# Kernel tuning notes

Measured on AMD Instinct MI355X. Metric: run time of the kernel, lower is better.

The kernel has to match this reference:

```python
import jax, jax.numpy as jnp
import numpy as np

N = 1024
C = 50000
D = 128
M_MARGIN = 0.35
S_SCALE = 30.0
LAMDA = 0.01


def setup_inputs() -> dict:
    key = jax.random.key(0)
    k1, k2, k3 = jax.random.split(key, 3)
    feature = jax.random.normal(k1, (N, D), dtype=jnp.float32)
    weight = jax.random.normal(k2, (C, D), dtype=jnp.float32)
    label = jax.random.randint(k3, (N,), 0, C, dtype=jnp.int64)
    return {"feature": feature, "weight": weight, "label": label}


def reference(feature, weight, label):
    eps = 1e-8  # torch CosineSimilarity eps
    f = feature / jnp.maximum(jnp.linalg.norm(feature, axis=-1, keepdims=True), eps)
    w = weight / jnp.maximum(jnp.linalg.norm(weight, axis=-1, keepdims=True), eps)
    cos = jnp.einsum("nd,cd->nc", f, w)  # [N, C] cosine similarities
    onehot = jax.nn.one_hot(label, C, dtype=cos.dtype)  # [N, C]
    # CosFace: subtract margin m from the target-class cosine, scale by s
    logits = S_SCALE * (cos - M_MARGIN * onehot)
    target_logit = S_SCALE * (jnp.take_along_axis(cos, label[:, None], axis=1)[:, 0] - M_MARGIN)
    # -log( exp(t) / (exp(t) + sum_{j != y} exp(s*cos_j)) ) = logsumexp(logits) - t
    lse = jax.nn.logsumexp(logits, axis=-1)  # [N]
    loss_lmc = jnp.mean(lse - target_logit)
    # center loss: 0.5 * sum_i ||f_i - w_{y_i}||^2
    diff = feature - weight[label]
    loss_c = 0.5 * jnp.sum(diff * diff)
    return loss_lmc + LAMDA * loss_c
```

## Files before the change

kernel.cpp:

```cpp
#include <hip/hip_runtime.h>

#define N_ROWS   1024
#define D_DIM    128
#define C_CLS    50000
#define C_PAD    50048
#define NCT64    782
#define NG       128
#define NPART    256
#define S_SCALE  30.0f
#define M_MARGIN 0.35f
#define EXP2_SCALE 43.2808512266689f
#define EXP2M      15.1482979293341f
#define LN2        0.6931471805599453f

typedef short s8v __attribute__((ext_vector_type(8)));
typedef float f4v __attribute__((ext_vector_type(4)));

__device__ inline unsigned short f2bf(float f) {
    unsigned u = __float_as_uint(f);
    u += 0x7FFF + ((u >> 16) & 1);
    return (unsigned short)(u >> 16);
}
__device__ inline float bf2f(unsigned short h) {
    return __uint_as_float(((unsigned)h) << 16);
}
__device__ inline void load_lds16(const char* src, unsigned char* lds) {
    __builtin_amdgcn_global_load_lds(
        (const __attribute__((address_space(1))) void*)src,
        (__attribute__((address_space(3))) void*)lds, 16, 0, 0);
}

__global__ void norm_rows_fused(const float* __restrict__ weight,
                                const float* __restrict__ feature,
                                unsigned short* __restrict__ what,
                                unsigned short* __restrict__ fhat) {
    int wid = threadIdx.x >> 6, lane = threadIdx.x & 63;
    int half = lane >> 5, l32 = lane & 31;
    int r = blockIdx.x * 8 + wid * 2 + half;

    const float* src;
    unsigned short* dst;
    int srcRow, valid;
    float scale;
    if (r < C_PAD) {
        src = weight; dst = what; srcRow = r; valid = (r < C_CLS); scale = 1.0f;
    } else {
        src = feature; dst = fhat; srcRow = r - C_PAD; valid = 1; scale = EXP2_SCALE;
    }
    float4 v = make_float4(0.f, 0.f, 0.f, 0.f);
    if (valid) v = ((const float4*)src)[(size_t)srcRow * 32 + l32];
    float ss = v.x * v.x + v.y * v.y + v.z * v.z + v.w * v.w;
    #pragma unroll
    for (int s = 1; s < 32; s <<= 1) ss += __shfl_xor(ss, s, 32);
    float inv = valid ? scale / fmaxf(sqrtf(ss), 1e-8f) : 0.f;
    ushort4 o;
    o.x = f2bf(v.x * inv); o.y = f2bf(v.y * inv);
    o.z = f2bf(v.z * inv); o.w = f2bf(v.w * inv);
    ((ushort4*)dst)[(size_t)srcRow * 32 + l32] = o;
}

__global__ __launch_bounds__(256, 3)
void gemm_exp_kernel(const short* __restrict__ fhat,
                     const short* __restrict__ what,
                     float* __restrict__ part2) {
    __shared__ __align__(16) unsigned char smem[32768];
    const int g   = blockIdx.x;
    const int rt  = blockIdx.y;
    const int tid = threadIdx.x;
    const int wid = tid >> 6;
    const int lane = tid & 63;
    const int lrow = lane & 15;
    const int kgrp = lane >> 4;
    const int wrow = wid >> 1;
    const int wcol = wid & 1;
    const int nt = (g < 14) ? 7 : 6;

    const char* aSrc  = (const char*)fhat + (size_t)rt * 32768;
    const char* bBase = (const char*)what;

    #pragma unroll
    for (int i = 0; i < 8; i++) {
        int o = wid * 8192 + i * 1024 + lane * 16;
        int s = o ^ (((o >> 8) & 7) << 4);
        load_lds16(aSrc + s, smem + o);
    }
    __syncthreads();

    s8v afr[4][4];
    #pragma unroll
    for (int kk = 0; kk < 4; kk++)
        #pragma unroll
        for (int m = 0; m < 4; m++) {
            int row = wrow * 64 + m * 16 + lrow;
            int b = (row * 256 + kk * 64 + kgrp * 16) ^ ((row & 7) << 4);
            afr[kk][m] = *(const s8v*)(smem + b);
        }
    __syncthreads();

    #pragma unroll
    for (int i = 0; i < 4; i++) {
        int o = wid * 4096 + i * 1024 + lane * 16;
        int s = o ^ (((o >> 8) & 7) << 4);
        load_lds16(bBase + (size_t)g * 16384 + s, smem + o);
    }

    float esum[4][4];
    #pragma unroll
    for (int m = 0; m < 4; m++)
        #pragma unroll
        for (int j = 0; j < 4; j++) esum[m][j] = 0.f;

    for (int t = 0; t < nt; ++t) {
        const int ct = g + 128 * t;
        __syncthreads();

        if (t + 1 < nt) {
            const char* src = bBase + (size_t)(ct + 128) * 16384;
            unsigned char* dstb = smem + ((t + 1) & 1) * 16384;
            #pragma unroll
            for (int i = 0; i < 4; i++) {
                int o = wid * 4096 + i * 1024 + lane * 16;
                int s = o ^ (((o >> 8) & 7) << 4);
                load_lds16(src + s, dstb + o);
            }
        }

        const unsigned char* bb = smem + (t & 1) * 16384;
        f4v acc[4][2];
        f4v zero = {0.f, 0.f, 0.f, 0.f};
        #pragma unroll
        for (int m = 0; m < 4; m++) { acc[m][0] = zero; acc[m][1] = zero; }

        #pragma unroll
        for (int kk = 0; kk < 4; kk++) {
            s8v bfr[2];
            #pragma unroll
            for (int n = 0; n < 2; n++) {
                int row = wcol * 32 + n * 16 + lrow;
                int b = (row * 256 + kk * 64 + kgrp * 16) ^ ((row & 7) << 4);
                bfr[n] = *(const s8v*)(bb + b);
            }
            #pragma unroll
            for (int m = 0; m < 4; m++) {
                acc[m][0] = __builtin_amdgcn_mfma_f32_16x16x32_bf16(
                    afr[kk][m], bfr[0], acc[m][0], 0, 0, 0);
                acc[m][1] = __builtin_amdgcn_mfma_f32_16x16x32_bf16(
                    afr[kk][m], bfr[1], acc[m][1], 0, 0, 0);
            }
        }

        if (ct != NCT64 - 1) {
            #pragma unroll
            for (int m = 0; m < 4; m++)
                #pragma unroll
                for (int n = 0; n < 2; n++)
                    #pragma unroll
                    for (int j = 0; j < 4; j++)
                        esum[m][j] += __builtin_amdgcn_exp2f(acc[m][n][j]);
        } else {
            #pragma unroll
            for (int n = 0; n < 2; n++) {
                int gc = ct * 64 + wcol * 32 + n * 16 + lrow;
                #pragma unroll
                for (int m = 0; m < 4; m++)
                    #pragma unroll
                    for (int j = 0; j < 4; j++)
                        if (gc < C_CLS)
                            esum[m][j] += __builtin_amdgcn_exp2f(acc[m][n][j]);
            }
        }
    }

    #pragma unroll
    for (int m = 0; m < 4; m++)
        #pragma unroll
        for (int j = 0; j < 4; j++) {
            float v = esum[m][j];
            v += __shfl_xor(v, 1, 64);
            v += __shfl_xor(v, 2, 64);
            v += __shfl_xor(v, 4, 64);
            v += __shfl_xor(v, 8, 64);
            if (lrow == 0) {
                int row = rt * 128 + wrow * 64 + m * 16 + kgrp * 4 + j;
                part2[(size_t)row * NPART + g * 2 + wcol] = v;
            }
        }
}

__global__ void finalize_rows_kernel(const float* __restrict__ part2,
                                     const unsigned short* __restrict__ fhat,
                                     const unsigned short* __restrict__ what,
                                     const float* __restrict__ feature,
                                     const float* __restrict__ weight,
                                     const int* __restrict__ label,
                                     float* __restrict__ rowval) {
    int wid = threadIdx.x >> 6, lane = threadIdx.x & 63;
    int n = blockIdx.x * 4 + wid;
    int y = label[n];

    const float* p = part2 + (size_t)n * NPART;
    float S = p[lane] + p[64 + lane] + p[128 + lane] + p[192 + lane];

    float2 f2 = ((const float2*)feature)[(size_t)n * 64 + lane];
    float2 w2 = ((const float2*)weight)[(size_t)y * 64 + lane];
    float dx = f2.x - w2.x, dy = f2.y - w2.y;
    float cl = dx * dx + dy * dy;

    ushort2 fh = ((const ushort2*)fhat)[(size_t)n * 64 + lane];
    ushort2 wh = ((const ushort2*)what)[(size_t)y * 64 + lane];
    float cys = bf2f(fh.x) * bf2f(wh.x) + bf2f(fh.y) * bf2f(wh.y);

    #pragma unroll
    for (int s = 1; s < 64; s <<= 1) {
        S   += __shfl_xor(S, s, 64);
        cl  += __shfl_xor(cl, s, 64);
        cys += __shfl_xor(cys, s, 64);
    }
    if (lane == 0) {
        float t2 = cys - EXP2M;
        float Sp = S - __builtin_amdgcn_exp2f(cys) + __builtin_amdgcn_exp2f(t2);
        rowval[n] = (logf(Sp) - LN2 * t2) * (1.0f / (float)N_ROWS) + 0.005f * cl;
    }
}

__global__ void reduce_final_kernel(const float* __restrict__ rowval, float* __restrict__ out) {
    __shared__ float sbuf[4];
    int t = threadIdx.x;
    float v = rowval[t] + rowval[t + 256] + rowval[t + 512] + rowval[t + 768];
    #pragma unroll
    for (int s = 1; s < 64; s <<= 1) v += __shfl_xor(v, s, 64);
    if ((t & 63) == 0) sbuf[t >> 6] = v;
    __syncthreads();
    if (t == 0) out[0] = sbuf[0] + sbuf[1] + sbuf[2] + sbuf[3];
}

extern "C" void kernel_launch(void* const* d_in, const int* in_sizes, int n_in,
                              void* d_out, int out_size, void* d_ws, size_t ws_size,
                              hipStream_t stream) {
    const float* feature = (const float*)d_in[0];
    const float* weight  = (const float*)d_in[1];
    const int*   label   = (const int*)d_in[2];

    const size_t WS_NEEDED = 14127104;
    if (ws_size < WS_NEEDED) return;

    char* ws = (char*)d_ws;
    unsigned short* what = (unsigned short*)ws;
    unsigned short* fhat = (unsigned short*)(ws + 12812288);
    float*         part2 = (float*)(ws + 13074432);
    float*        rowval = (float*)(ws + 14123008);

    norm_rows_fused<<<dim3((C_PAD + N_ROWS) / 8), 256, 0, stream>>>(weight, feature, what, fhat);
    gemm_exp_kernel<<<dim3(NG, 8), 256, 0, stream>>>((const short*)fhat, (const short*)what, part2);
    finalize_rows_kernel<<<dim3(N_ROWS / 4), 256, 0, stream>>>(part2, fhat, what, feature, weight,
                                                               label, rowval);
    reduce_final_kernel<<<1, 256, 0, stream>>>(rowval, (float*)d_out);
}
```

Measured before the change: 36.00 us.

## Deepen weight-tile prefetch to a 4-buffer ring with larger 256-row blocks

The GEMM+exp kernel now runs 512-thread blocks that each cover 256 feature rows instead of 128, which halves the grid and the number of times each weight tile is re-streamed. Weight tiles move through a 4-slot LDS ring with three tiles in flight, using explicit vmcnt waits and raw s_barrier instead of __syncthreads. The tile loop is fully unrolled through a template. In exchange it uses 64KB of LDS per block and needs more registers per block, which may cut occupancy. The hand-written wait counts are fragile to any change in how many loads are issued.

```diff
diff --git a/kernel.cpp b/kernel.cpp
--- a/kernel.cpp
+++ b/kernel.cpp
@@ -13,6 +13,10 @@
 #define EXP2M      15.1482979293341f
 #define LN2        0.6931471805599453f
 
+#define VM4 asm volatile("s_waitcnt vmcnt(4)" ::: "memory")
+#define VM2 asm volatile("s_waitcnt vmcnt(2)" ::: "memory")
+#define VM0 asm volatile("s_waitcnt vmcnt(0)" ::: "memory")
+
 typedef short s8v __attribute__((ext_vector_type(8)));
 typedef float f4v __attribute__((ext_vector_type(4)));
 
@@ -59,13 +63,76 @@
     ((ushort4*)dst)[(size_t)srcRow * 32 + l32] = o;
 }
 
-__global__ __launch_bounds__(256, 3)
+template<int I>
+__device__ __forceinline__ void gemm_body(
+    unsigned char* __restrict__ smem, const char* __restrict__ bSrc,
+    int sOffL, int dOff, const int (&vb)[2][4], const s8v (&afr)[4][4],
+    float (&esum)[4][4], int g, int nt, int wcol, int lrow)
+{
+    constexpr int BUFO  = (I & 3) * 16384;
+    constexpr int SBUFO = ((I + 3) & 3) * 16384;
+
+    if constexpr (I <= 3)      { VM4; }
+    else if constexpr (I == 4) { if (nt == 7) { VM4; } else { VM2; } }
+    else if constexpr (I == 5) { if (nt == 7) { VM2; } else { VM0; } }
+    else                       { VM0; }
+    __builtin_amdgcn_s_barrier();
+    __builtin_amdgcn_sched_barrier(0);
+
+    if constexpr (I <= 3) {
+        if (I <= 2 || nt == 7) {
+            const char* src = bSrc + (size_t)(I + 3) * 2097152;
+            load_lds16(src + sOffL,        smem + SBUFO + dOff);
+            load_lds16(src + sOffL + 8192, smem + SBUFO + dOff + 8192);
+        }
+    }
+
+    f4v acc[4][2];
+    f4v zero = {0.f, 0.f, 0.f, 0.f};
+    #pragma unroll
+    for (int m = 0; m < 4; m++) { acc[m][0] = zero; acc[m][1] = zero; }
+
+    #pragma unroll
+    for (int kk = 0; kk < 4; kk++) {
+        s8v b0 = *(const s8v*)(smem + BUFO + vb[0][kk]);
+        s8v b1 = *(const s8v*)(smem + BUFO + vb[1][kk]);
+        #pragma unroll
+        for (int m = 0; m < 4; m++) {
+            acc[m][0] = __builtin_amdgcn_mfma_f32_16x16x32_bf16(afr[kk][m], b0, acc[m][0], 0, 0, 0);
+            acc[m][1] = __builtin_amdgcn_mfma_f32_16x16x32_bf16(afr[kk][m], b1, acc[m][1], 0, 0, 0);
+        }
+    }
+
+    const int ct = g + 128 * I;
+    if (ct != NCT64 - 1) {
+        #pragma unroll
+        for (int m = 0; m < 4; m++)
+            #pragma unroll
+            for (int n = 0; n < 2; n++)
+                #pragma unroll
+                for (int j = 0; j < 4; j++)
+                    esum[m][j] += __builtin_amdgcn_exp2f(acc[m][n][j]);
+    } else {
+        #pragma unroll
+        for (int n = 0; n < 2; n++) {
+            int gc = ct * 64 + wcol * 32 + n * 16 + lrow;
+            #pragma unroll
+            for (int m = 0; m < 4; m++)
+                #pragma unroll
+                for (int j = 0; j < 4; j++)
+                    if (gc < C_CLS)
+                        esum[m][j] += __builtin_amdgcn_exp2f(acc[m][n][j]);
+        }
+    }
+}
+
+__global__ __launch_bounds__(512, 4)
 void gemm_exp_kernel(const short* __restrict__ fhat,
                      const short* __restrict__ what,
                      float* __restrict__ part2) {
-    __shared__ __align__(16) unsigned char smem[32768];
+    __shared__ __align__(16) unsigned char smem[65536];
     const int g   = blockIdx.x;
-    const int rt  = blockIdx.y;
+    const int rt2 = blockIdx.y;
     const int tid = threadIdx.x;
     const int wid = tid >> 6;
     const int lane = tid & 63;
@@ -75,8 +142,8 @@
     const int wcol = wid & 1;
     const int nt = (g < 14) ? 7 : 6;
 
-    const char* aSrc  = (const char*)fhat + (size_t)rt * 32768;
-    const char* bBase = (const char*)what;
+    const char* aSrc = (const char*)fhat + (size_t)rt2 * 65536;
+    const char* bSrc = (const char*)what + (size_t)g * 16384;
 
     #pragma unroll
     for (int i = 0; i < 8; i++) {
@@ -97,11 +164,22 @@
         }
     __syncthreads();
 
-    #pragma unroll
-    for (int i = 0; i < 4; i++) {
-        int o = wid * 4096 + i * 1024 + lane * 16;
-        int s = o ^ (((o >> 8) & 7) << 4);
-        load_lds16(bBase + (size_t)g * 16384 + s, smem + o);
+    const int dOff  = wid * 1024 + lane * 16;
+    const int sOffL = dOff ^ (((dOff >> 8) & 7) << 4);
+    int vb[2][4];
+    #pragma unroll
+    for (int n = 0; n < 2; n++)
+        #pragma unroll
+        for (int kk = 0; kk < 4; kk++) {
+            int row = wcol * 32 + n * 16 + lrow;
+            vb[n][kk] = (row * 256 + kk * 64 + kgrp * 16) ^ ((row & 7) << 4);
+        }
+
+    #pragma unroll
+    for (int tt = 0; tt < 3; ++tt) {
+        const char* src = bSrc + (size_t)tt * 2097152;
+        load_lds16(src + sOffL,        smem + tt * 16384 + dOff);
+        load_lds16(src + sOffL + 8192, smem + tt * 16384 + dOff + 8192);
     }
 
     float esum[4][4];
@@ -110,66 +188,14 @@
         #pragma unroll
         for (int j = 0; j < 4; j++) esum[m][j] = 0.f;
 
-    for (int t = 0; t < nt; ++t) {
-        const int ct = g + 128 * t;
-        __syncthreads();
-
-        if (t + 1 < nt) {
-            const char* src = bBase + (size_t)(ct + 128) * 16384;
-            unsigned char* dstb = smem + ((t + 1) & 1) * 16384;
-            #pragma unroll
-            for (int i = 0; i < 4; i++) {
-                int o = wid * 4096 + i * 1024 + lane * 16;
-                int s = o ^ (((o >> 8) & 7) << 4);
-                load_lds16(src + s, dstb + o);
-            }
-        }
-
-        const unsigned char* bb = smem + (t & 1) * 16384;
-        f4v acc[4][2];
-        f4v zero = {0.f, 0.f, 0.f, 0.f};
-        #pragma unroll
-        for (int m = 0; m < 4; m++) { acc[m][0] = zero; acc[m][1] = zero; }
-
-        #pragma unroll
-        for (int kk = 0; kk < 4; kk++) {
-            s8v bfr[2];
-            #pragma unroll
-            for (int n = 0; n < 2; n++) {
-                int row = wcol * 32 + n * 16 + lrow;
-                int b = (row * 256 + kk * 64 + kgrp * 16) ^ ((row & 7) << 4);
-                bfr[n] = *(const s8v*)(bb + b);
-            }
-            #pragma unroll
-            for (int m = 0; m < 4; m++) {
-                acc[m][0] = __builtin_amdgcn_mfma_f32_16x16x32_bf16(
-                    afr[kk][m], bfr[0], acc[m][0], 0, 0, 0);
-                acc[m][1] = __builtin_amdgcn_mfma_f32_16x16x32_bf16(
-                    afr[kk][m], bfr[1], acc[m][1], 0, 0, 0);
-            }
-        }
-
-        if (ct != NCT64 - 1) {
-            #pragma unroll
-            for (int m = 0; m < 4; m++)
-                #pragma unroll
-                for (int n = 0; n < 2; n++)
-                    #pragma unroll
-                    for (int j = 0; j < 4; j++)
-                        esum[m][j] += __builtin_amdgcn_exp2f(acc[m][n][j]);
-        } else {
-            #pragma unroll
-            for (int n = 0; n < 2; n++) {
-                int gc = ct * 64 + wcol * 32 + n * 16 + lrow;
-                #pragma unroll
-                for (int m = 0; m < 4; m++)
-                    #pragma unroll
-                    for (int j = 0; j < 4; j++)
-                        if (gc < C_CLS)
-                            esum[m][j] += __builtin_amdgcn_exp2f(acc[m][n][j]);
-            }
-        }
-    }
+    gemm_body<0>(smem, bSrc, sOffL, dOff, vb, afr, esum, g, nt, wcol, lrow);
+    gemm_body<1>(smem, bSrc, sOffL, dOff, vb, afr, esum, g, nt, wcol, lrow);
+    gemm_body<2>(smem, bSrc, sOffL, dOff, vb, afr, esum, g, nt, wcol, lrow);
+    gemm_body<3>(smem, bSrc, sOffL, dOff, vb, afr, esum, g, nt, wcol, lrow);
+    gemm_body<4>(smem, bSrc, sOffL, dOff, vb, afr, esum, g, nt, wcol, lrow);
+    gemm_body<5>(smem, bSrc, sOffL, dOff, vb, afr, esum, g, nt, wcol, lrow);
+    if (nt == 7)
+        gemm_body<6>(smem, bSrc, sOffL, dOff, vb, afr, esum, g, nt, wcol, lrow);
 
     #pragma unroll
     for (int m = 0; m < 4; m++)
@@ -181,7 +207,7 @@
             v += __shfl_xor(v, 4, 64);
             v += __shfl_xor(v, 8, 64);
             if (lrow == 0) {
-                int row = rt * 128 + wrow * 64 + m * 16 + kgrp * 4 + j;
+                int row = rt2 * 256 + wrow * 64 + m * 16 + kgrp * 4 + j;
                 part2[(size_t)row * NPART + g * 2 + wcol] = v;
             }
         }
@@ -251,7 +277,7 @@
     float*        rowval = (float*)(ws + 14123008);
 
     norm_rows_fused<<<dim3((C_PAD + N_ROWS) / 8), 256, 0, stream>>>(weight, feature, what, fhat);
-    gemm_exp_kernel<<<dim3(NG, 8), 256, 0, stream>>>((const short*)fhat, (const short*)what, part2);
+    gemm_exp_kernel<<<dim3(NG, 4), 512, 0, stream>>>((const short*)fhat, (const short*)what, part2);
     finalize_rows_kernel<<<dim3(N_ROWS / 4), 256, 0, stream>>>(part2, fhat, what, feature, weight,
                                                                label, rowval);
     reduce_final_kernel<<<1, 256, 0, stream>>>(rowval, (float*)d_out);
```

Measured after the change: 53.70 us. 1.49x slower.
